# Optimization experiments

Measured on AMD Instinct MI355X. Metric: run time of the kernel, lower is better.

The kernel has to match this reference:

```python
import jax, jax.numpy as jnp
import numpy as np

B, T, D = 4, 2048, 1024
EPS = 1e-5


def _layernorm(x, g, b):
    mu = jnp.mean(x, axis=-1, keepdims=True)
    var = jnp.var(x, axis=-1, keepdims=True)
    return (x - mu) * jax.lax.rsqrt(var + EPS) * g + b


def setup_inputs() -> dict:
    key = jax.random.key(0)
    ks = jax.random.split(key, 16)
    s = lambda fan_in: 1.0 / np.sqrt(fan_in)
    return {
        "x": jax.random.normal(ks[0], (B, T, D), dtype=jnp.float32),
        "ln1_g": jnp.ones((D,), jnp.float32),
        "ln1_b": jnp.zeros((D,), jnp.float32),
        "Wqkv": jax.random.uniform(ks[1], (D, 3 * D), jnp.float32, -s(D), s(D)),
        "bqkv": jnp.zeros((3 * D,), jnp.float32),
        "Wproj": jax.random.uniform(ks[2], (D, D), jnp.float32, -s(D), s(D)),
        "bproj": jnp.zeros((D,), jnp.float32),
        "ln2_g": jnp.ones((D,), jnp.float32),
        "ln2_b": jnp.zeros((D,), jnp.float32),
        "W1": jax.random.uniform(ks[3], (D, 4 * D), jnp.float32, -s(D), s(D)),
        "b1": jnp.zeros((4 * D,), jnp.float32),
        "W2": jax.random.uniform(ks[4], (4 * D, D), jnp.float32, -s(4 * D), s(4 * D)),
        "b2": jnp.zeros((D,), jnp.float32),
    }


def reference(x, ln1_g, ln1_b, Wqkv, bqkv, Wproj, bproj, ln2_g, ln2_b, W1, b1, W2, b2):
    # NOTE: no residual connections in the original Block.
    h = _layernorm(x, ln1_g, ln1_b)
    kqv = h @ Wqkv + bqkv                      # [B,T,3D]
    k, q, v = jnp.split(kqv, 3, axis=-1)       # split order: k, q, v
    # Original scales by 1/sqrt(k.size(-1)) AFTER transposing k -> 1/sqrt(T).
    scores = jnp.einsum("btd,bsd->bts", q, k) * (1.0 / np.sqrt(T))
    causal = jnp.tril(jnp.ones((T, T), dtype=bool))
    scores = jnp.where(causal, scores, -jnp.inf)
    attn = jax.nn.softmax(scores, axis=-1)
    a = jnp.einsum("bts,bsd->btd", attn, v)
    a = a @ Wproj + bproj
    h2 = _layernorm(a, ln2_g, ln2_b)
    m = jax.nn.gelu(h2 @ W1 + b1, approximate=True)
    return m @ W2 + b2
```

## Files before the change

### kernel.cpp

```cpp
#include <hip/hip_runtime.h>
#include <hip/hip_bf16.h>

typedef __hip_bfloat16 bf16;
typedef __bf16 bf16x8 __attribute__((ext_vector_type(8)));
typedef __bf16 bf16x4 __attribute__((ext_vector_type(4)));
typedef __bf16 bf16x2 __attribute__((ext_vector_type(2)));
typedef float f32x4 __attribute__((ext_vector_type(4)));

static constexpr int Bq = 4, Tq = 2048, Dq = 1024;

__device__ inline float b2f(bf16 h) { return __bfloat162float(h); }
__device__ inline bf16 f2b(float f) { return __float2bfloat16(f); }

__device__ __forceinline__ void gload_lds16(const bf16* g, bf16* lds_wave_base) {
    __builtin_amdgcn_global_load_lds((const __attribute__((address_space(1))) void*)g,
                                     (__attribute__((address_space(3))) void*)lds_wave_base,
                                     16, 0, 0);
}

__device__ __forceinline__ float fast_gelu(float x) {
    float u = x * (0.7978845608028654f + 0.03567740814183427f * x * x);
    float e = __builtin_amdgcn_exp2f(-2.885390081777927f * u);
    return x * __builtin_amdgcn_rcpf(1.f + e);
}

__device__ inline void ld4f(const float* p, float* v) {
    float4 t = *reinterpret_cast<const float4*>(p);
    v[0] = t.x; v[1] = t.y; v[2] = t.z; v[3] = t.w;
}
__device__ inline void ld4f(const bf16* p, float* v) {
    bf16x4 t = *reinterpret_cast<const bf16x4*>(p);
    v[0] = (float)t[0]; v[1] = (float)t[1]; v[2] = (float)t[2]; v[3] = (float)t[3];
}

template <typename Tin>
__device__ __forceinline__ void ln_body(const Tin* __restrict__ x, const float* __restrict__ g,
                                        const float* __restrict__ b, bf16* __restrict__ out,
                                        int row, float* sred)
{
    const int tid = threadIdx.x;
    const int s0 = tid * 4;
    const Tin* xr = x + (size_t)row * Dq;
    bf16* orow = out + (size_t)row * Dq;
    float v[4], gv[4], bv[4];
    ld4f(xr + s0, v);
    ld4f(g + s0, gv);
    ld4f(b + s0, bv);
    float sum = v[0] + v[1] + v[2] + v[3];
    float sq = v[0]*v[0] + v[1]*v[1] + v[2]*v[2] + v[3]*v[3];
    for (int o = 32; o > 0; o >>= 1) { sum += __shfl_xor(sum, o); sq += __shfl_xor(sq, o); }
    const int w = tid >> 6;
    if ((tid & 63) == 0) { sred[w] = sum; sred[4 + w] = sq; }
    __syncthreads();
    const float ts = sred[0] + sred[1] + sred[2] + sred[3];
    const float tq = sred[4] + sred[5] + sred[6] + sred[7];
    const float mean = ts / Dq;
    const float rs = rsqrtf(tq / Dq - mean * mean + 1e-5f);
    bf16x4 o4;
    #pragma unroll
    for (int i = 0; i < 4; ++i) o4[i] = (__bf16)((v[i] - mean) * rs * gv[i] + bv[i]);
    *reinterpret_cast<bf16x4*>(orow + s0) = o4;
}

__global__ void ln_kernel(const bf16* __restrict__ x, const float* __restrict__ g,
                          const float* __restrict__ b, bf16* __restrict__ out)
{
    __shared__ float sred[8];
    ln_body(x, g, b, out, blockIdx.x, sred);
}

__global__ void prep_kernel(const float* __restrict__ x, const float* __restrict__ g,
                            const float* __restrict__ b, bf16* __restrict__ h,
                            const float* __restrict__ Wqkv, bf16* __restrict__ WqkvT,
                            const float* __restrict__ Wproj, bf16* __restrict__ WprojT,
                            const float* __restrict__ W1, bf16* __restrict__ W1T,
                            const float* __restrict__ W2, bf16* __restrict__ W2T)
{
    __shared__ float smem[64 * 65];
    int id = blockIdx.x;
    if (id < 8192) { ln_body(x, g, b, h, id, smem); return; }
    id -= 8192;
    const float* src; bf16* dst; long ldin, ldout; int gx;
    if (id < 768)       { src = Wqkv;  dst = WqkvT;  ldin = 3072; ldout = 1024; gx = 48; }
    else if (id < 1024) { id -= 768;  src = Wproj; dst = WprojT; ldin = 1024; ldout = 1024; gx = 16; }
    else if (id < 2048) { id -= 1024; src = W1;    dst = W1T;    ldin = 4096; ldout = 1024; gx = 64; }
    else                { id -= 2048; src = W2;    dst = W2T;    ldin = 1024; ldout = 4096; gx = 16; }
    const int c0 = (id % gx) * 64, r0 = (id / gx) * 64;
    const int tid = threadIdx.x;
    const int tx = tid & 63, ty = tid >> 6;
    float (*tile)[65] = reinterpret_cast<float(*)[65]>(smem);
    #pragma unroll
    for (int i = 0; i < 16; ++i) {
        int r = ty + i * 4;
        tile[r][tx] = src[(size_t)(r0 + r) * ldin + c0 + tx];
    }
    __syncthreads();
    const int px = tid & 31, cy = tid >> 5;
    #pragma unroll
    for (int i = 0; i < 8; ++i) {
        int cc = cy + i * 8;
        bf16x2 p;
        p[0] = (__bf16)tile[px * 2][cc];
        p[1] = (__bf16)tile[px * 2 + 1][cc];
        *reinterpret_cast<bf16x2*>(&dst[(size_t)(c0 + cc) * ldout + r0 + px * 2]) = p;
    }
}

template <int ACT, int TRI, int CK, int FR>
__global__ void gemm128(const bf16* __restrict__ A, const bf16* __restrict__ Bt,
                        const float* __restrict__ bias,
                        bf16* __restrict__ Cb, float* __restrict__ Cf,
                        int K, long lda, long ldb, long ldc,
                        long sA, long sB, long sC, float scale,
                        const bf16* __restrict__ vsrc, bf16* __restrict__ vdst)
{
    __shared__ bf16 As[128 * 64];
    __shared__ bf16 Bs[128 * 64];

    int bx, by;
    if (TRI) {
        const int lin = blockIdx.x;
        if (lin >= 136) {
            const int idx = lin - 136;
            const int c0 = (idx & 15) * 64, r0 = (idx >> 4) * 64;
            const bf16* ip = vsrc + (size_t)blockIdx.z * ((size_t)Tq * 3072);
            bf16* op = vdst + (size_t)blockIdx.z * ((size_t)Dq * Tq);
            bf16 (*tile)[66] = reinterpret_cast<bf16(*)[66]>(As);
            const int tid = threadIdx.x;
            const int tx = tid & 31, ty = tid >> 5;
            #pragma unroll
            for (int i = 0; i < 8; ++i) {
                int r = ty + i * 8;
                *reinterpret_cast<bf16x2*>(&tile[r][tx * 2]) =
                    *reinterpret_cast<const bf16x2*>(&ip[(size_t)(r0 + r) * 3072 + c0 + tx * 2]);
            }
            __syncthreads();
            #pragma unroll
            for (int i = 0; i < 8; ++i) {
                int cc = ty + i * 8;
                bf16x2 p;
                p[0] = tile[tx * 2][cc];
                p[1] = tile[tx * 2 + 1][cc];
                *reinterpret_cast<bf16x2*>(&op[(size_t)(c0 + cc) * 2048 + r0 + tx * 2]) = p;
            }
            return;
        }
        int t = (int)((sqrtf(8.f * lin + 1.f) - 1.f) * 0.5f);
        while ((t + 1) * (t + 2) / 2 <= lin) ++t;
        while (t * (t + 1) / 2 > lin) --t;
        by = t; bx = lin - t * (t + 1) / 2;
    } else {
        const int gx = gridDim.x, gy = gridDim.y;
        const int lin = blockIdx.x + gx * blockIdx.y;
        const int band = lin & 7;
        const int idx = lin >> 3;
        bx = idx % gx;
        by = band * (gy >> 3) + idx / gx;
    }

    const int m0 = by * 128, n0 = bx * 128;
    const int Kend = CK ? min(K, m0 + 128) : K;

    const bf16* Ab = A + (size_t)blockIdx.z * sA;
    const bf16* Bb = Bt + (size_t)blockIdx.z * sB;
    const int tid = threadIdx.x;
    const int wid = tid >> 6, lane = tid & 63;
    const int wr = wid >> 1, wc = wid & 1;
    const int l15 = lane & 15, quad = lane >> 4;

    const int rloc = lane >> 3, slot = lane & 7;
    const bf16* agp = Ab + (size_t)(m0 + wid * 32 + rloc) * lda + (slot ^ rloc) * 8;
    const bf16* bgp = Bb + (size_t)(n0 + wid * 32 + rloc) * ldb + (slot ^ rloc) * 8;
    bf16* awb = As + wid * 32 * 64;
    bf16* bwb = Bs + wid * 32 * 64;

    const int afo = (wr * 64 + l15) * 64 + ((quad ^ (l15 & 7)) * 8);
    const int bfo = (wc * 64 + l15) * 64 + ((quad ^ (l15 & 7)) * 8);

    f32x4 acc[4][4];
    #pragma unroll
    for (int i = 0; i < 4; ++i)
        #pragma unroll
        for (int j = 0; j < 4; ++j) acc[i][j] = (f32x4){0.f, 0.f, 0.f, 0.f};

    f32x4 acc_l[4];
    bf16x8 ones;
    if (FR) {
        #pragma unroll
        for (int i = 0; i < 4; ++i) acc_l[i] = (f32x4){0.f, 0.f, 0.f, 0.f};
        #pragma unroll
        for (int i = 0; i < 8; ++i) ones[i] = (__bf16)1.0f;
    }

    for (int k0 = 0; k0 < Kend; k0 += 64) {
        #pragma unroll
        for (int i = 0; i < 4; ++i) {
            gload_lds16(agp + k0 + (size_t)(i * 8) * lda, awb + i * 8 * 64);
            gload_lds16(bgp + k0 + (size_t)(i * 8) * ldb, bwb + i * 8 * 64);
        }
        __syncthreads();

        bf16x8 af0[4], bf0[4], af1[4], bf1[4];
        #pragma unroll
        for (int i = 0; i < 4; ++i) {
            af0[i] = *reinterpret_cast<const bf16x8*>(As + (afo ^ 0)  + i * 1024);
            af1[i] = *reinterpret_cast<const bf16x8*>(As + (afo ^ 32) + i * 1024);
        }
        #pragma unroll
        for (int j = 0; j < 4; ++j) {
            bf0[j] = *reinterpret_cast<const bf16x8*>(Bs + (bfo ^ 0)  + j * 1024);
            bf1[j] = *reinterpret_cast<const bf16x8*>(Bs + (bfo ^ 32) + j * 1024);
        }
        #pragma unroll
        for (int i = 0; i < 4; ++i)
            #pragma unroll
            for (int j = 0; j < 4; ++j)
                acc[i][j] = __builtin_amdgcn_mfma_f32_16x16x32_bf16(af0[i], bf0[j], acc[i][j], 0, 0, 0);
        if (FR) {
            #pragma unroll
            for (int i = 0; i < 4; ++i)
                acc_l[i] = __builtin_amdgcn_mfma_f32_16x16x32_bf16(af0[i], ones, acc_l[i], 0, 0, 0);
        }
        #pragma unroll
        for (int i = 0; i < 4; ++i)
            #pragma unroll
            for (int j = 0; j < 4; ++j)
                acc[i][j] = __builtin_amdgcn_mfma_f32_16x16x32_bf16(af1[i], bf1[j], acc[i][j], 0, 0, 0);
        if (FR) {
            #pragma unroll
            for (int i = 0; i < 4; ++i)
                acc_l[i] = __builtin_amdgcn_mfma_f32_16x16x32_bf16(af1[i], ones, acc_l[i], 0, 0, 0);
        }

        __syncthreads();
    }

    #pragma unroll
    for (int i = 0; i < 4; ++i) {
        const int row = m0 + wr * 64 + i * 16 + quad * 4;
        #pragma unroll
        for (int j = 0; j < 4; ++j) {
            const int col = n0 + wc * 64 + j * 16 + l15;
            const float bv = bias ? bias[col] : 0.f;
            #pragma unroll
            for (int r = 0; r < 4; ++r) {
                float vv = scale * acc[i][j][r] + bv;
                if (ACT == 1) vv = fast_gelu(vv);
                else if (ACT == 2)
                    vv = (col <= row + r) ? __builtin_amdgcn_exp2f(1.4426950408889634f * vv) : 0.f;
                if (FR) vv *= __builtin_amdgcn_rcpf(acc_l[i][r]);
                const size_t idx2 = (size_t)(row + r) * ldc + col + (size_t)blockIdx.z * sC;
                if (Cf) Cf[idx2] = vv;
                else    Cb[idx2] = f2b(vv);
            }
        }
    }
}

template <int ACT>
__global__ __launch_bounds__(512) void gemm256(
        const bf16* __restrict__ A, const bf16* __restrict__ Bt,
        const float* __restrict__ bias, bf16* __restrict__ C,
        int K, long lda, long ldb, long ldc)
{
    __shared__ bf16 As[2][256 * 64];
    __shared__ bf16 Bs[2][256 * 64];

    const int gx = gridDim.x, gy = gridDim.y;
    const int lin = blockIdx.x + gx * blockIdx.y;
    const int band = lin & 7;
    const int idx = lin >> 3;
    const int bx = idx % gx;
    const int by = band * (gy >> 3) + idx / gx;
    const int m0 = by * 256, n0 = bx * 256;

    const int tid = threadIdx.x;
    const int wid = tid >> 6, lane = tid & 63;
    const int wr = wid >> 2, wc = wid & 3;
    const int l15 = lane & 15, quad = lane >> 4;
    const int rloc = lane >> 3, slot = lane & 7;

    const bf16* agp = A + (size_t)(m0 + wid * 8 + rloc) * lda + (slot ^ rloc) * 8;
    const bf16* bgp = Bt + (size_t)(n0 + wid * 8 + rloc) * ldb + (slot ^ rloc) * 8;

    auto issueA = [&](int buf, int t2, int R) {
        gload_lds16(agp + (size_t)R * lda + t2 * 64, &As[buf][(R + wid * 8) * 64]);
    };
    auto issueB = [&](int buf, int t2, int R) {
        gload_lds16(bgp + (size_t)R * ldb + t2 * 64, &Bs[buf][(R + wid * 8) * 64]);
    };

    const int xg = (quad ^ (l15 & 7)) * 8;
    const int afo = (wr * 128 + l15) * 64 + xg;
    const int bfo = (wc * 64 + l15) * 64 + xg;

    f32x4 acc[8][4];
    #pragma unroll
    for (int i = 0; i < 8; ++i)
        #pragma unroll
        for (int j = 0; j < 4; ++j) acc[i][j] = (f32x4){0.f, 0.f, 0.f, 0.f};

    bf16x8 aA[4], aB[4], B0[4], B1[4];

    const int nt = K >> 6;

#define RD_A(buf, rh, ks, dst)                                                            \
    { _Pragma("unroll")                                                                   \
      for (int i_ = 0; i_ < 4; ++i_)                                                      \
          dst[i_] = *reinterpret_cast<const bf16x8*>(                                     \
              &As[buf][(afo + (rh) * 4096 + i_ * 1024) ^ ((ks) * 32)]); }
#define RD_B(buf, ks, dst)                                                                \
    { _Pragma("unroll")                                                                   \
      for (int j_ = 0; j_ < 4; ++j_)                                                      \
          dst[j_] = *reinterpret_cast<const bf16x8*>(                                     \
              &Bs[buf][(bfo + j_ * 1024) ^ ((ks) * 32)]); }
#define MF8(rh, Aset, Bset, I0)                                                           \
    { __builtin_amdgcn_s_setprio(1);                                                      \
      _Pragma("unroll")                                                                   \
      for (int i_ = (I0); i_ < (I0) + 2; ++i_)                                            \
          _Pragma("unroll")                                                               \
          for (int j_ = 0; j_ < 4; ++j_)                                                  \
              acc[(rh) * 4 + i_][j_] = __builtin_amdgcn_mfma_f32_16x16x32_bf16(           \
                  Aset[i_], Bset[j_], acc[(rh) * 4 + i_][j_], 0, 0, 0);                   \
      __builtin_amdgcn_s_setprio(0); }
#define STAGE8(buf, t2)                                                                   \
    { issueA(buf, t2, 0); issueA(buf, t2, 64); issueA(buf, t2, 128); issueA(buf, t2, 192);\
      issueB(buf, t2, 0); issueB(buf, t2, 64); issueB(buf, t2, 128); issueB(buf, t2, 192); }
#define BAR()    __builtin_amdgcn_s_barrier()
#define CFENCE() asm volatile("" ::: "memory")
#define VMCNT0() asm volatile("s_waitcnt vmcnt(0)" ::: "memory")

    STAGE8(0, 0);
    VMCNT0();
    CFENCE(); BAR(); CFENCE();

#define TILE_BODY(bp, bq, tn, PRE)                                                        \
    RD_A(bp, 0, 0, aA); RD_B(bp, 0, B0); RD_B(bp, 1, B1);                                 \
    MF8(0, aA, B0, 0);                                                                    \
    RD_A(bp, 0, 1, aB);                                                                   \
    MF8(0, aA, B0, 2);                                                                    \
    MF8(0, aB, B1, 0);                                                                    \
    RD_A(bp, 1, 0, aA);                                                                   \
    if (PRE) STAGE8(bq, tn);                                                              \
    MF8(0, aB, B1, 2);                                                                    \
    MF8(1, aA, B0, 0);                                                                    \
    RD_A(bp, 1, 1, aB);                                                                   \
    MF8(1, aA, B0, 2);                                                                    \
    MF8(1, aB, B1, 0);                                                                    \
    MF8(1, aB, B1, 2);                                                                    \
    VMCNT0();                                                                             \
    CFENCE(); BAR(); CFENCE();

    for (int t = 0; t < nt; t += 2) {
        TILE_BODY(0, 1, t + 1, true);
        const bool pre2 = (t + 2) < nt;
        TILE_BODY(1, 0, t + 2, pre2);
    }
#undef TILE_BODY
#undef RD_A
#undef RD_B
#undef MF8
#undef STAGE8
#undef BAR
#undef CFENCE
#undef VMCNT0

    #pragma unroll
    for (int i = 0; i < 8; ++i) {
        const int row = m0 + wr * 128 + i * 16 + quad * 4;
        #pragma unroll
        for (int j = 0; j < 4; ++j) {
            const int col = n0 + wc * 64 + j * 16 + l15;
            const float bv = bias ? bias[col] : 0.f;
            #pragma unroll
            for (int r = 0; r < 4; ++r) {
                float vv = acc[i][j][r] + bv;
                if (ACT == 1) vv = fast_gelu(vv);
                C[(size_t)(row + r) * ldc + col] = f2b(vv);
            }
        }
    }
}

template <int ACT>
__global__ __launch_bounds__(512) void gemm128x256(
        const bf16* __restrict__ A, const bf16* __restrict__ Bt,
        const float* __restrict__ bias,
        bf16* __restrict__ Cb, float* __restrict__ Cf,
        int K, long lda, long ldb, long ldc)
{
    __shared__ bf16 As[2][128 * 64];
    __shared__ bf16 Bs[2][256 * 64];

    const int gx = gridDim.x, gy = gridDim.y;
    const int lin = blockIdx.x + gx * blockIdx.y;
    const int band = lin & 7;
    const int idx = lin >> 3;
    const int bx = idx % gx;
    const int by = band * (gy >> 3) + idx / gx;
    const int m0 = by * 128, n0 = bx * 256;

    const int tid = threadIdx.x;
    const int wid = tid >> 6, lane = tid & 63;
    const int wr = wid >> 2, wc = wid & 3;
    const int l15 = lane & 15, quad = lane >> 4;
    const int rloc = lane >> 3, slot = lane & 7;

    const bf16* agp = A + (size_t)(m0 + wid * 8 + rloc) * lda + (slot ^ rloc) * 8;
    const bf16* bgp = Bt + (size_t)(n0 + wid * 8 + rloc) * ldb + (slot ^ rloc) * 8;

    auto issueA = [&](int buf, int t2, int R) {
        gload_lds16(agp + (size_t)R * lda + t2 * 64, &As[buf][(R + wid * 8) * 64]);
    };
    auto issueB = [&](int buf, int t2, int R) {
        gload_lds16(bgp + (size_t)R * ldb + t2 * 64, &Bs[buf][(R + wid * 8) * 64]);
    };

    const int xg = (quad ^ (l15 & 7)) * 8;
    const int afo = (wr * 64 + l15) * 64 + xg;
    const int bfo = (wc * 64 + l15) * 64 + xg;

    f32x4 acc[4][4];
    #pragma unroll
    for (int i = 0; i < 4; ++i)
        #pragma unroll
        for (int j = 0; j < 4; ++j) acc[i][j] = (f32x4){0.f, 0.f, 0.f, 0.f};

    bf16x8 aA[4], aB[4], B0[4], B1[4];

    const int nt = K >> 6;

#define RD_A(buf, ks, dst)                                                                \
    { _Pragma("unroll")                                                                   \
      for (int i_ = 0; i_ < 4; ++i_)                                                      \
          dst[i_] = *reinterpret_cast<const bf16x8*>(                                     \
              &As[buf][(afo + i_ * 1024) ^ ((ks) * 32)]); }
#define RD_B(buf, ks, dst)                                                                \
    { _Pragma("unroll")                                                                   \
      for (int j_ = 0; j_ < 4; ++j_)                                                      \
          dst[j_] = *reinterpret_cast<const bf16x8*>(                                     \
              &Bs[buf][(bfo + j_ * 1024) ^ ((ks) * 32)]); }
#define MF8(Aset, Bset, I0)                                                               \
    { __builtin_amdgcn_s_setprio(1);                                                      \
      _Pragma("unroll")                                                                   \
      for (int i_ = (I0); i_ < (I0) + 2; ++i_)                                            \
          _Pragma("unroll")                                                               \
          for (int j_ = 0; j_ < 4; ++j_)                                                  \
              acc[i_][j_] = __builtin_amdgcn_mfma_f32_16x16x32_bf16(                      \
                  Aset[i_], Bset[j_], acc[i_][j_], 0, 0, 0);                              \
      __builtin_amdgcn_s_setprio(0); }
#define STAGE6(buf, t2)                                                                   \
    { issueA(buf, t2, 0); issueA(buf, t2, 64);                                            \
      issueB(buf, t2, 0); issueB(buf, t2, 64); issueB(buf, t2, 128); issueB(buf, t2, 192); }
#define BAR()    __builtin_amdgcn_s_barrier()
#define CFENCE() asm volatile("" ::: "memory")
#define VMCNT0() asm volatile("s_waitcnt vmcnt(0)" ::: "memory")

    STAGE6(0, 0);
    VMCNT0();
    CFENCE(); BAR(); CFENCE();

#define TILE_BODY(bp, bq, tn, PRE)                                                        \
    RD_A(bp, 0, aA); RD_B(bp, 0, B0);                                                     \
    MF8(aA, B0, 0);                                                                       \
    RD_A(bp, 1, aB); RD_B(bp, 1, B1);                                                     \
    MF8(aA, B0, 2);                                                                       \
    if (PRE) STAGE6(bq, tn);                                                              \
    MF8(aB, B1, 0);                                                                       \
    MF8(aB, B1, 2);                                                                       \
    VMCNT0();                                                                             \
    CFENCE(); BAR(); CFENCE();

    for (int t = 0; t < nt; t += 2) {
        TILE_BODY(0, 1, t + 1, true);
        const bool pre2 = (t + 2) < nt;
        TILE_BODY(1, 0, t + 2, pre2);
    }
#undef TILE_BODY
#undef RD_A
#undef RD_B
#undef MF8
#undef STAGE6
#undef BAR
#undef CFENCE
#undef VMCNT0

    #pragma unroll
    for (int i = 0; i < 4; ++i) {
        const int row = m0 + wr * 64 + i * 16 + quad * 4;
        #pragma unroll
        for (int j = 0; j < 4; ++j) {
            const int col = n0 + wc * 64 + j * 16 + l15;
            const float bv = bias ? bias[col] : 0.f;
            #pragma unroll
            for (int r = 0; r < 4; ++r) {
                float vv = acc[i][j][r] + bv;
                if (ACT == 1) vv = fast_gelu(vv);
                const size_t idx2 = (size_t)(row + r) * ldc + col;
                if (Cf) Cf[idx2] = vv;
                else    Cb[idx2] = f2b(vv);
            }
        }
    }
}

extern "C" void kernel_launch(void* const* d_in, const int* in_sizes, int n_in,
                              void* d_out, int out_size, void* d_ws, size_t ws_size,
                              hipStream_t stream)
{
    (void)in_sizes; (void)n_in; (void)out_size; (void)ws_size;
    const float* x     = (const float*)d_in[0];
    const float* ln1g  = (const float*)d_in[1];
    const float* ln1b  = (const float*)d_in[2];
    const float* Wqkv  = (const float*)d_in[3];
    const float* bqkv  = (const float*)d_in[4];
    const float* Wproj = (const float*)d_in[5];
    const float* bproj = (const float*)d_in[6];
    const float* ln2g  = (const float*)d_in[7];
    const float* ln2b  = (const float*)d_in[8];
    const float* W1    = (const float*)d_in[9];
    const float* b1    = (const float*)d_in[10];
    const float* W2    = (const float*)d_in[11];
    const float* b2    = (const float*)d_in[12];
    float* out = (float*)d_out;

    char* ws = (char*)d_ws;
    size_t off = 0;
    auto alloc = [&](size_t elems) { bf16* p = (bf16*)(ws + off); off += elems * sizeof(bf16); return p; };
    bf16* WqkvT  = alloc(3072UL * 1024);
    bf16* WprojT = alloc(1024UL * 1024);
    bf16* W1T    = alloc(4096UL * 1024);
    bf16* W2T    = alloc(1024UL * 4096);
    bf16* h      = alloc(8192UL * 1024);
    bf16* kqv    = alloc(8192UL * 3072);
    bf16* vT     = alloc(4UL * 1024 * 2048);
    bf16* attn   = alloc(4UL * 2048 * 2048);
    bf16* a   = h;
    bf16* p   = kqv;
    bf16* h2  = kqv + 8192UL * 1024;
    bf16* m   = kqv + 2UL * 8192 * 1024;

    const long T3D = (long)Tq * 3072, TT = (long)Tq * Tq, DT = (long)Dq * Tq, TD = (long)Tq * Dq;

    prep_kernel<<<11264, 256, 0, stream>>>(x, ln1g, ln1b, h,
                                           Wqkv, WqkvT, Wproj, WprojT, W1, W1T, W2, W2T);

    gemm256<0><<<dim3(12, 32, 1), 512, 0, stream>>>(h, WqkvT, bqkv, kqv,
        1024, 1024L, 1024L, 3072L);

    gemm128<2,1,0,0><<<dim3(648, 1, 4), 256, 0, stream>>>(kqv + 1024, kqv, nullptr, attn, nullptr,
        1024, 3072L, 3072L, 2048L, T3D, T3D, TT, 0.022097086912079608f, kqv + 2048, vT);

    gemm128<0,0,1,1><<<dim3(8, 16, 4), 256, 0, stream>>>(attn, vT, nullptr, a, nullptr,
        2048, 2048L, 2048L, 1024L, TT, DT, TD, 1.f, nullptr, nullptr);

    gemm128x256<0><<<dim3(4, 64, 1), 512, 0, stream>>>(a, WprojT, bproj, p, nullptr,
        1024, 1024L, 1024L, 1024L);

    ln_kernel<<<8192, 256, 0, stream>>>(p, ln2g, ln2b, h2);

    gemm256<1><<<dim3(16, 32, 1), 512, 0, stream>>>(h2, W1T, b1, m,
        1024, 1024L, 1024L, 4096L);

    gemm128x256<0><<<dim3(4, 64, 1), 512, 0, stream>>>(m, W2T, b2, nullptr, out,
        4096, 4096L, 4096L, 1024L);
}
```

Measured before the change: 466.4 us.

## Add 4-stage K32 pipelined GEMM for MLP up-projection; reverse causal PV block order

Adds a new 256x256 GEMM kernel that uses K-steps of 32 with a four-buffer LDS ring, prefetching three stages ahead and interleaving fragment reads with MFMA issue. It replaces the previous gemm256 for the W1+GELU projection. Separately, the causal attention-times-V GEMM now walks row blocks in reverse, so the longest-K (bottom) tiles launch first and the work tail is shorter. The new kernel uses more LDS and a more complex wait/barrier schedule.

```diff
diff --git a/kernel.cpp b/kernel.cpp
--- a/kernel.cpp
+++ b/kernel.cpp
@@ -106,7 +106,7 @@
     }
 }
 
-template <int ACT, int TRI, int CK, int FR>
+template <int ACT, int TRI, int CK, int FR, int RV>
 __global__ void gemm128(const bf16* __restrict__ A, const bf16* __restrict__ Bt,
                         const float* __restrict__ bias,
                         bf16* __restrict__ Cb, float* __restrict__ Cf,
@@ -156,6 +156,7 @@
         const int idx = lin >> 3;
         bx = idx % gx;
         by = band * (gy >> 3) + idx / gx;
+        if (RV) by = gy - 1 - by;
     }
 
     const int m0 = by * 128, n0 = bx * 128;
@@ -504,6 +505,125 @@
     }
 }
 
+template <int ACT>
+__global__ __launch_bounds__(512) void gemm256k32(
+        const bf16* __restrict__ A, const bf16* __restrict__ Bt,
+        const float* __restrict__ bias, bf16* __restrict__ C,
+        int K, long lda, long ldb, long ldc)
+{
+    __shared__ bf16 As[4][256 * 32];
+    __shared__ bf16 Bs[4][256 * 32];
+
+    const int gx = gridDim.x, gy = gridDim.y;
+    const int lin = blockIdx.x + gx * blockIdx.y;
+    const int band = lin & 7;
+    const int idx = lin >> 3;
+    const int bx = idx % gx;
+    const int by = band * (gy >> 3) + idx / gx;
+    const int m0 = by * 256, n0 = bx * 256;
+
+    const int tid = threadIdx.x;
+    const int wid = tid >> 6, lane = tid & 63;
+    const int wr = wid >> 2, wc = wid & 3;
+    const int l15 = lane & 15, quad = lane >> 4;
+
+    const int srow = lane >> 2, sslot = lane & 3;
+    const int sgran = sslot ^ ((lane >> 3) & 3);
+    const bf16* agp = A + (size_t)(m0 + wid * 16 + srow) * lda + sgran * 8;
+    const bf16* bgp = Bt + (size_t)(n0 + wid * 16 + srow) * ldb + sgran * 8;
+
+    auto issueA = [&](int buf, int t2, int R) {
+        gload_lds16(agp + (size_t)R * lda + t2 * 32, &As[buf][(R + wid * 16) * 32]);
+    };
+    auto issueB = [&](int buf, int t2, int R) {
+        gload_lds16(bgp + (size_t)R * ldb + t2 * 32, &Bs[buf][(R + wid * 16) * 32]);
+    };
+
+    const int swz8 = (quad ^ ((l15 >> 1) & 3)) * 8;
+    const int afo = (wr * 128 + l15) * 32 + swz8;
+    const int bfo = (wc * 64 + l15) * 32 + swz8;
+
+    f32x4 acc[8][4];
+    #pragma unroll
+    for (int i = 0; i < 8; ++i)
+        #pragma unroll
+        for (int j = 0; j < 4; ++j) acc[i][j] = (f32x4){0.f, 0.f, 0.f, 0.f};
+
+    bf16x8 Af[4], Ao[4], Bc[4], Bn[4];
+
+    const int nt = K >> 5;
+
+#define RD_A4(buf, I0, dst)                                                               \
+    { _Pragma("unroll")                                                                   \
+      for (int i_ = 0; i_ < 4; ++i_)                                                      \
+          dst[i_] = *reinterpret_cast<const bf16x8*>(&As[buf][afo + ((I0) + i_) * 512]); }
+#define RD_B4(buf, dst)                                                                   \
+    { _Pragma("unroll")                                                                   \
+      for (int j_ = 0; j_ < 4; ++j_)                                                      \
+          dst[j_] = *reinterpret_cast<const bf16x8*>(&Bs[buf][bfo + j_ * 512]); }
+#define MF16(I0, Aset, Bset)                                                              \
+    { __builtin_amdgcn_s_setprio(1);                                                      \
+      _Pragma("unroll")                                                                   \
+      for (int i_ = 0; i_ < 4; ++i_)                                                      \
+          _Pragma("unroll")                                                               \
+          for (int j_ = 0; j_ < 4; ++j_)                                                  \
+              acc[(I0) + i_][j_] = __builtin_amdgcn_mfma_f32_16x16x32_bf16(               \
+                  Aset[i_], Bset[j_], acc[(I0) + i_][j_], 0, 0, 0);                       \
+      __builtin_amdgcn_s_setprio(0); }
+#define STAGE4(buf, t2)                                                                   \
+    { issueA(buf, t2, 0); issueA(buf, t2, 128); issueB(buf, t2, 0); issueB(buf, t2, 128); }
+#define BAR()    __builtin_amdgcn_s_barrier()
+#define CFENCE() asm volatile("" ::: "memory")
+
+    STAGE4(0, 0); STAGE4(1, 1); STAGE4(2, 2);
+    asm volatile("s_waitcnt vmcnt(4)" ::: "memory");
+    CFENCE(); BAR(); CFENCE();
+    RD_B4(0, Bc);
+    RD_A4(0, 0, Af);
+
+#define TILE32(bT, bT1, bS, t, Bcur, Bnxt)                                                \
+    { const bool PRE = (t) + 3 < nt;                                                      \
+      RD_A4(bT, 4, Ao);                                    \
+      MF16(0, Af, Bcur);                             \
+      RD_B4(bT1, Bnxt);                            \
+      RD_A4(bT1, 0, Af);                                \
+      if (PRE) STAGE4(bS, (t) + 3);                                                       \
+      MF16(4, Ao, Bcur);                                                  \
+      if (PRE) { asm volatile("s_waitcnt vmcnt(4)" ::: "memory"); }                       \
+      else     { asm volatile("s_waitcnt vmcnt(0)" ::: "memory"); }                       \
+      CFENCE(); BAR(); CFENCE(); }
+
+    for (int t = 0; t < nt; t += 4) {
+        TILE32(0, 1, 3, t + 0, Bc, Bn);
+        TILE32(1, 2, 0, t + 1, Bn, Bc);
+        TILE32(2, 3, 1, t + 2, Bc, Bn);
+        TILE32(3, 0, 2, t + 3, Bn, Bc);
+    }
+#undef TILE32
+#undef RD_A4
+#undef RD_B4
+#undef MF16
+#undef STAGE4
+#undef BAR
+#undef CFENCE
+
+    #pragma unroll
+    for (int i = 0; i < 8; ++i) {
+        const int row = m0 + wr * 128 + i * 16 + quad * 4;
+        #pragma unroll
+        for (int j = 0; j < 4; ++j) {
+            const int col = n0 + wc * 64 + j * 16 + l15;
+            const float bv = bias ? bias[col] : 0.f;
+            #pragma unroll
+            for (int r = 0; r < 4; ++r) {
+                float vv = acc[i][j][r] + bv;
+                if (ACT == 1) vv = fast_gelu(vv);
+                C[(size_t)(row + r) * ldc + col] = f2b(vv);
+            }
+        }
+    }
+}
+
 extern "C" void kernel_launch(void* const* d_in, const int* in_sizes, int n_in,
                               void* d_out, int out_size, void* d_ws, size_t ws_size,
                               hipStream_t stream)
@@ -548,10 +668,10 @@
     gemm256<0><<<dim3(12, 32, 1), 512, 0, stream>>>(h, WqkvT, bqkv, kqv,
         1024, 1024L, 1024L, 3072L);
 
-    gemm128<2,1,0,0><<<dim3(648, 1, 4), 256, 0, stream>>>(kqv + 1024, kqv, nullptr, attn, nullptr,
+    gemm128<2,1,0,0,0><<<dim3(648, 1, 4), 256, 0, stream>>>(kqv + 1024, kqv, nullptr, attn, nullptr,
         1024, 3072L, 3072L, 2048L, T3D, T3D, TT, 0.022097086912079608f, kqv + 2048, vT);
 
-    gemm128<0,0,1,1><<<dim3(8, 16, 4), 256, 0, stream>>>(attn, vT, nullptr, a, nullptr,
+    gemm128<0,0,1,1,1><<<dim3(8, 16, 4), 256, 0, stream>>>(attn, vT, nullptr, a, nullptr,
         2048, 2048L, 2048L, 1024L, TT, DT, TD, 1.f, nullptr, nullptr);
 
     gemm128x256<0><<<dim3(4, 64, 1), 512, 0, stream>>>(a, WprojT, bproj, p, nullptr,
@@ -559,7 +679,7 @@
 
     ln_kernel<<<8192, 256, 0, stream>>>(p, ln2g, ln2b, h2);
 
-    gemm256<1><<<dim3(16, 32, 1), 512, 0, stream>>>(h2, W1T, b1, m,
+    gemm256k32<1><<<dim3(16, 32, 1), 512, 0, stream>>>(h2, W1T, b1, m,
         1024, 1024L, 1024L, 4096L);
 
     gemm128x256<0><<<dim3(4, 64, 1), 512, 0, stream>>>(m, W2T, b2, nullptr, out,
```

Measured after the change: 477.5 us. 2.4% more time.
